# Performance work log

Hardware: AMD Instinct MI355X
Metric: run time of the kernel (lower is better)

Reference implementation:

```python
import jax, jax.numpy as jnp
import numpy as np

N_EMBD = 768
N_HEAD = 12
HEAD_DIM = N_EMBD // N_HEAD


def setup_inputs() -> dict:
    key = jax.random.key(0)
    k1, k2, k3, k4, k5 = jax.random.split(key, 5)
    B, T, C = 8, 1024, N_EMBD
    s = 0.02
    return {
        "x": jax.random.normal(k1, (B, T, C), dtype=jnp.float32),
        "w_attn": jax.random.normal(k2, (C, 3 * C), dtype=jnp.float32) * s,
        "b_attn": jnp.zeros((3 * C,), dtype=jnp.float32),
        "w_proj": jax.random.normal(k3, (C, C), dtype=jnp.float32) * s,
        "b_proj": jnp.zeros((C,), dtype=jnp.float32),
    }


def reference(x, w_attn, b_attn, w_proj, b_proj):
    B, T, C = x.shape
    H, D = N_HEAD, HEAD_DIM
    qkv = x @ w_attn + b_attn                      # [B,T,3C]
    q, k, v = jnp.split(qkv, 3, axis=-1)
    # [B,H,T,D]
    q = q.reshape(B, T, H, D).transpose(0, 2, 1, 3)
    k = k.reshape(B, T, H, D).transpose(0, 2, 1, 3)
    v = v.reshape(B, T, H, D).transpose(0, 2, 1, 3)
    att = jnp.einsum("bhqd,bhkd->bhqk", q, k) / jnp.sqrt(jnp.float32(D))
    causal = jnp.tril(jnp.ones((T, T), dtype=bool))
    att = jnp.where(causal[None, None], att, jnp.float32(-jnp.inf))
    att = jax.nn.softmax(att, axis=-1)
    y = jnp.einsum("bhqk,bhkd->bhqd", att, v)      # [B,H,T,D]
    y = y.transpose(0, 2, 1, 3).reshape(B, T, C)
    return y @ w_proj + b_proj
```

## Files before the change

kernel.cpp:

```cpp
#include <hip/hip_runtime.h>
#include <hip/hip_bf16.h>
#include <math.h>
#include <type_traits>

#define BATCH 8
#define SEQ   1024
#define NEMBD 768
#define NHEAD 12
#define HDIM  64
#define TC    (3 * NEMBD)

typedef __attribute__((ext_vector_type(4))) float f32x4;
typedef __attribute__((ext_vector_type(8))) short s16x8;

__device__ __forceinline__ unsigned short f2bf(float f) {
    return __builtin_bit_cast(unsigned short, __float2bfloat16(f));
}

__device__ __forceinline__ void gload_lds16(const void* g, void* l) {
    __builtin_amdgcn_global_load_lds(
        (const __attribute__((address_space(1))) void*)g,
        (__attribute__((address_space(3))) void*)l, 16, 0, 0);
}

__global__ __launch_bounds__(256) void cast_bf16_kernel(
    const float* __restrict__ in, unsigned short* __restrict__ out, int n)
{
    const int i = (blockIdx.x * 256 + threadIdx.x) * 8;
    float4 a = *(const float4*)(in + i);
    float4 b = *(const float4*)(in + i + 4);
    s16x8 v;
    v[0] = f2bf(a.x); v[1] = f2bf(a.y); v[2] = f2bf(a.z); v[3] = f2bf(a.w);
    v[4] = f2bf(b.x); v[5] = f2bf(b.y); v[6] = f2bf(b.z); v[7] = f2bf(b.w);
    *(s16x8*)(out + i) = v;
}

__global__ __launch_bounds__(256) void transpose_cast_kernel(
    const float* __restrict__ w, unsigned short* __restrict__ wT, int K, int N)
{
    __shared__ float t[32][33];
    const int tx = threadIdx.x, ty = threadIdx.y;
    const int n0 = blockIdx.x * 32, k0 = blockIdx.y * 32;
    #pragma unroll
    for (int i = 0; i < 4; ++i)
        t[ty + i * 8][tx] = w[(size_t)(k0 + ty + i * 8) * N + n0 + tx];
    __syncthreads();
    #pragma unroll
    for (int i = 0; i < 4; ++i)
        wT[(size_t)(n0 + ty + i * 8) * K + k0 + tx] = f2bf(t[tx][ty + i * 8]);
}

__global__ __launch_bounds__(256) void gemm_proj_kernel(
    const unsigned short* __restrict__ A,
    const unsigned short* __restrict__ Bt,
    const float* __restrict__ bias,
    float* __restrict__ C,
    int M, int N, int K, int nbn)
{
    constexpr int BUF = 16384;
    __shared__ __align__(16) char SM[3 * BUF];

    const int tid  = threadIdx.x;
    const int w    = tid >> 6, lane = tid & 63;
    const int lr   = lane & 15, lg = lane >> 4;
    const int wr   = w >> 1, wc = w & 1;

    const int swz = (blockIdx.x & 7) * (gridDim.x >> 3) + (blockIdx.x >> 3);
    const int bm = (swz / nbn) * 128, bn = (swz % nbn) * 128;

    const int srow = tid >> 2;
    const int gcol = ((tid & 3) ^ ((srow >> 1) & 3)) * 8;
    const unsigned short* Ag = A  + (size_t)(bm + srow) * K + gcol;
    const unsigned short* Bg = Bt + (size_t)(bn + srow) * K + gcol;

    const int NT = K >> 5;

    f32x4 acc[4][4];
    #pragma unroll
    for (int m = 0; m < 4; ++m)
        #pragma unroll
        for (int n = 0; n < 4; ++n) acc[m][n] = (f32x4){0.f, 0.f, 0.f, 0.f};

    auto stage = [&](int t) {
        const int k0 = t << 5;
        char* buf = SM + (t % 3) * BUF;
        #pragma unroll
        for (int p = 0; p < 2; ++p)
            gload_lds16(Ag + (size_t)(p * 64) * K + k0, buf + p * 4096 + tid * 16);
        #pragma unroll
        for (int p = 0; p < 2; ++p)
            gload_lds16(Bg + (size_t)(p * 64) * K + k0,
                        buf + 8192 + p * 4096 + tid * 16);
    };

    stage(0);
    stage(1);
    asm volatile("s_waitcnt vmcnt(4)" ::: "memory");
    __builtin_amdgcn_sched_barrier(0);
    __builtin_amdgcn_s_barrier();
    __builtin_amdgcn_sched_barrier(0);

    for (int t = 0; t < NT; ++t) {
        const char* buf = SM + (t % 3) * BUF;
        const bool more = (t + 2 < NT);
        if (more) stage(t + 2);

        s16x8 af[4], bfr[4];
        #pragma unroll
        for (int m = 0; m < 4; ++m) {
            const int ar = wr * 64 + m * 16 + lr;
            af[m] = *(const s16x8*)(buf + ar * 64 + ((lg ^ ((ar >> 1) & 3)) * 16));
        }
        #pragma unroll
        for (int n = 0; n < 4; ++n) {
            const int br = wc * 64 + n * 16 + lr;
            bfr[n] = *(const s16x8*)(buf + 8192 + br * 64
                                         + ((lg ^ ((br >> 1) & 3)) * 16));
        }

        __builtin_amdgcn_s_setprio(1);
        #pragma unroll
        for (int m = 0; m < 4; ++m)
            #pragma unroll
            for (int n = 0; n < 4; ++n)
                acc[m][n] = __builtin_amdgcn_mfma_f32_16x16x32_bf16(
                    af[m], bfr[n], acc[m][n], 0, 0, 0);
        __builtin_amdgcn_s_setprio(0);

        if (more) asm volatile("s_waitcnt vmcnt(4)" ::: "memory");
        else      asm volatile("s_waitcnt vmcnt(0)" ::: "memory");
        __builtin_amdgcn_sched_barrier(0);
        __builtin_amdgcn_s_barrier();
        __builtin_amdgcn_sched_barrier(0);
    }

    #pragma unroll
    for (int n = 0; n < 4; ++n) {
        const int col = bn + wc * 64 + n * 16 + lr;
        const float bv = bias[col];
        #pragma unroll
        for (int m = 0; m < 4; ++m) {
            const int row0 = bm + wr * 64 + m * 16 + lg * 4;
            #pragma unroll
            for (int r = 0; r < 4; ++r)
                C[(size_t)(row0 + r) * N + col] = acc[m][n][r] + bv;
        }
    }
}

__global__ __launch_bounds__(512) void gemm_qkv256_kernel(
    const unsigned short* __restrict__ A,
    const unsigned short* __restrict__ Bt,
    const float* __restrict__ bias,
    unsigned short* __restrict__ Qb,
    unsigned short* __restrict__ Kb,
    unsigned short* __restrict__ Vtb,
    int M, int K, int nbn)
{
    constexpr int BUF = 24576;
    __shared__ __align__(16) char SM[3 * BUF];

    const int tid  = threadIdx.x;
    const int w    = tid >> 6, lane = tid & 63;
    const int lr   = lane & 15, lg = lane >> 4;
    const int wr   = w >> 1, wc = w & 1;

    const int swz = (blockIdx.x & 7) * (gridDim.x >> 3) + (blockIdx.x >> 3);
    const int bm = (swz / nbn) * 256, bn = (swz % nbn) * 128;

    const int srow = tid >> 2;
    const int gcol = ((tid & 3) ^ ((srow >> 1) & 3)) * 8;
    const unsigned short* Ag = A  + (size_t)(bm + srow) * K + gcol;
    const unsigned short* Bg = Bt + (size_t)(bn + srow) * K + gcol;

    const int NT = K >> 5;

    f32x4 acc[4][4];
    #pragma unroll
    for (int m = 0; m < 4; ++m)
        #pragma unroll
        for (int n = 0; n < 4; ++n) acc[m][n] = (f32x4){0.f, 0.f, 0.f, 0.f};

    auto stage = [&](int t) {
        const int k0 = t << 5;
        char* buf = SM + (t % 3) * BUF;
        gload_lds16(Ag + k0,                        buf + tid * 16);
        gload_lds16(Ag + (size_t)128 * K + k0,      buf + 8192 + tid * 16);
        gload_lds16(Bg + k0,                        buf + 16384 + tid * 16);
    };

    stage(0);
    stage(1);
    asm volatile("s_waitcnt vmcnt(3)" ::: "memory");
    __builtin_amdgcn_sched_barrier(0);
    __builtin_amdgcn_s_barrier();
    __builtin_amdgcn_sched_barrier(0);

    for (int t = 0; t < NT; ++t) {
        const char* buf = SM + (t % 3) * BUF;
        const bool more = (t + 2 < NT);
        if (more) stage(t + 2);

        s16x8 af[4], bfr[4];
        #pragma unroll
        for (int m = 0; m < 4; ++m) {
            const int ar = wr * 64 + m * 16 + lr;
            af[m] = *(const s16x8*)(buf + ar * 64 + ((lg ^ ((ar >> 1) & 3)) * 16));
        }
        #pragma unroll
        for (int n = 0; n < 4; ++n) {
            const int br = wc * 64 + n * 16 + lr;
            bfr[n] = *(const s16x8*)(buf + 16384 + br * 64
                                         + ((lg ^ ((br >> 1) & 3)) * 16));
        }

        __builtin_amdgcn_s_setprio(1);
        #pragma unroll
        for (int m = 0; m < 4; ++m)
            #pragma unroll
            for (int n = 0; n < 4; ++n)
                acc[m][n] = __builtin_amdgcn_mfma_f32_16x16x32_bf16(
                    af[m], bfr[n], acc[m][n], 0, 0, 0);
        __builtin_amdgcn_s_setprio(0);

        if (more) asm volatile("s_waitcnt vmcnt(3)" ::: "memory");
        else      asm volatile("s_waitcnt vmcnt(0)" ::: "memory");
        __builtin_amdgcn_sched_barrier(0);
        __builtin_amdgcn_s_barrier();
        __builtin_amdgcn_sched_barrier(0);
    }

    char* Ep = SM + w * 8192;

    const int region = bn / NEMBD;
    const int hh = ((bn % NEMBD) >> 6) + wc;
    const int row0 = bm + wr * 64;
    const int bb = row0 >> 10, t0 = row0 & 1023;
    const float scl = (region == 0) ? 0.1803368801111354f : 1.0f;

    float bvn[4];
    #pragma unroll
    for (int n = 0; n < 4; ++n) bvn[n] = bias[bn + wc * 64 + n * 16 + lr];

    if (region == 2) {
        #pragma unroll
        for (int m = 0; m < 4; ++m)
            #pragma unroll
            for (int n = 0; n < 4; ++n) {
                ushort4 pk;
                pk.x = f2bf(acc[m][n][0] + bvn[n]);
                pk.y = f2bf(acc[m][n][1] + bvn[n]);
                pk.z = f2bf(acc[m][n][2] + bvn[n]);
                pk.w = f2bf(acc[m][n][3] + bvn[n]);
                const int row = n * 16 + lr;
                const int lc  = m * 2 + (lg >> 1);
                *(ushort4*)(Ep + row * 128 + ((lc ^ (lr & 7)) * 16)
                               + (lg & 1) * 8) = pk;
            }
    } else {
        #pragma unroll
        for (int m = 0; m < 4; ++m)
            #pragma unroll
            for (int n = 0; n < 4; ++n)
                #pragma unroll
                for (int r = 0; r < 4; ++r) {
                    const int row = m * 16 + lg * 4 + r;
                    const int lc  = n * 2 + (lr >> 3);
                    *(unsigned short*)(Ep + row * 128
                        + ((lc ^ (row & 7)) * 16) + (lr & 7) * 2) =
                        f2bf((acc[m][n][r] + bvn[n]) * scl);
                }
    }
    asm volatile("s_waitcnt lgkmcnt(0)" ::: "memory");
    __builtin_amdgcn_sched_barrier(0);

    const int rr0 = lane >> 3;
    const int cc  = lane & 7;
    if (region == 2) {
        unsigned short* dst = Vtb + (((size_t)bb * NHEAD + hh) * HDIM) * SEQ + t0;
        #pragma unroll
        for (int it = 0; it < 8; ++it) {
            const int d = it * 8 + rr0;
            s16x8 v = *(const s16x8*)(Ep + d * 128 + ((cc ^ (d & 7)) * 16));
            *(s16x8*)(dst + (size_t)d * SEQ + cc * 8) = v;
        }
    } else {
        unsigned short* dst = (region == 0 ? Qb : Kb)
                            + ((size_t)bb * NHEAD + hh) * SEQ * HDIM;
        #pragma unroll
        for (int it = 0; it < 8; ++it) {
            const int t = it * 8 + rr0;
            s16x8 v = *(const s16x8*)(Ep + t * 128 + ((cc ^ (t & 7)) * 16));
            *(s16x8*)(dst + (size_t)(t0 + t) * HDIM + cc * 8) = v;
        }
    }
}

__global__ __launch_bounds__(256) void attn_mfma_kernel(
    const unsigned short* __restrict__ Qb,
    const unsigned short* __restrict__ Kb,
    const unsigned short* __restrict__ Vtb,
    unsigned short* __restrict__ y)
{
    const int bid  = blockIdx.x;
    const int xcd  = bid & 7;
    const int grp  = bid >> 3;
    const int pair = grp & 7;
    const int bh   = xcd + 8 * (grp >> 3);
    const int b    = bh / NHEAD, h = bh % NHEAD;

    const int tid  = threadIdx.x;
    const int w    = tid >> 6;
    const int lane = tid & 63;
    const int lr   = lane & 15;
    const int lg   = lane >> 4;

    __shared__ __align__(16) unsigned short Ks[64 * 72];
    __shared__ __align__(16) unsigned short Vs[64 * 72];
    __shared__ __align__(16) unsigned short Ps[4][16][72];

    const unsigned short* Kg = Kb  + (size_t)bh * SEQ * HDIM;
    const unsigned short* Vg = Vtb + (size_t)bh * HDIM * SEQ;

    const int sr = tid >> 2;
    const int sc = (tid & 3) * 16;
    const unsigned short* Kgr = Kg + (size_t)sr * HDIM + sc;
    const unsigned short* Vgr = Vg + (size_t)sr * SEQ  + sc;
    unsigned short* KsW = Ks + sr * 72 + sc;
    unsigned short* VsW = Vs + sr * 72 + sc;

    auto process = [&](int qt) {
        const unsigned short* Qg =
            Qb + ((size_t)bh * SEQ + qt * 64 + w * 16) * HDIM;
        s16x8 qf[2];
        #pragma unroll
        for (int kc = 0; kc < 2; ++kc)
            qf[kc] = *(const s16x8*)(Qg + (size_t)lr * HDIM + kc * 32 + lg * 8);

        f32x4 acc[4];
        #pragma unroll
        for (int df = 0; df < 4; ++df) acc[df] = (f32x4){0.f, 0.f, 0.f, 0.f};
        float mrow = -INFINITY, lrow = 0.f;

        const int NT   = qt + 1;
        const int qrow = qt * 64 + w * 16 + lr;

        s16x8 krA = *(const s16x8*)(Kgr);
        s16x8 krB = *(const s16x8*)(Kgr + 8);
        s16x8 vrA = *(const s16x8*)(Vgr);
        s16x8 vrB = *(const s16x8*)(Vgr + 8);

        for (int kt = 0; kt < NT; ++kt) {
            __syncthreads();
            *(s16x8*)(KsW)     = krA;
            *(s16x8*)(KsW + 8) = krB;
            *(s16x8*)(VsW)     = vrA;
            *(s16x8*)(VsW + 8) = vrB;
            __syncthreads();
            if (kt + 1 < NT) {
                krA = *(const s16x8*)(Kgr + (size_t)(kt + 1) * 64 * HDIM);
                krB = *(const s16x8*)(Kgr + (size_t)(kt + 1) * 64 * HDIM + 8);
                vrA = *(const s16x8*)(Vgr + (kt + 1) * 64);
                vrB = *(const s16x8*)(Vgr + (kt + 1) * 64 + 8);
            }

            f32x4 sf[4];
            __builtin_amdgcn_s_setprio(1);
            #pragma unroll
            for (int s = 0; s < 4; ++s) {
                const unsigned short* kr = &Ks[(s * 16 + lr) * 72 + lg * 8];
                s16x8 a0 = *(const s16x8*)(kr);
                s16x8 a1 = *(const s16x8*)(kr + 32);
                sf[s] = __builtin_amdgcn_mfma_f32_16x16x32_bf16(
                    a0, qf[0], (f32x4){0.f, 0.f, 0.f, 0.f}, 0, 0, 0);
                sf[s] = __builtin_amdgcn_mfma_f32_16x16x32_bf16(a1, qf[1], sf[s], 0, 0, 0);
            }
            __builtin_amdgcn_s_setprio(0);

            float sv[4][4];
            #pragma unroll
            for (int s = 0; s < 4; ++s)
                #pragma unroll
                for (int r = 0; r < 4; ++r)
                    sv[s][r] = sf[s][r];
            if (kt == NT - 1) {
                const int kbase = kt * 64;
                #pragma unroll
                for (int s = 0; s < 4; ++s)
                    #pragma unroll
                    for (int r = 0; r < 4; ++r)
                        if (kbase + s * 16 + lg * 4 + r > qrow)
                            sv[s][r] = -INFINITY;
            }

            float mx4[4];
            #pragma unroll
            for (int s = 0; s < 4; ++s)
                mx4[s] = fmaxf(fmaxf(sv[s][0], sv[s][1]), fmaxf(sv[s][2], sv[s][3]));
            float mx = fmaxf(fmaxf(mx4[0], mx4[1]), fmaxf(mx4[2], mx4[3]));
            mx = fmaxf(mx, __shfl_xor(mx, 16, 64));
            mx = fmaxf(mx, __shfl_xor(mx, 32, 64));
            if (!__all(mx - mrow <= 8.f)) {
                const float mnew = fmaxf(mrow, mx);
                const float al   = exp2f(mrow - mnew);
                lrow *= al;
                #pragma unroll
                for (int df = 0; df < 4; ++df) acc[df] *= al;
                mrow = mnew;
            }

            float rsum = 0.f;
            #pragma unroll
            for (int s = 0; s < 4; ++s) {
                float p0 = exp2f(sv[s][0] - mrow);
                float p1 = exp2f(sv[s][1] - mrow);
                float p2 = exp2f(sv[s][2] - mrow);
                float p3 = exp2f(sv[s][3] - mrow);
                rsum += (p0 + p1) + (p2 + p3);
                ushort4 pk;
                pk.x = f2bf(p0); pk.y = f2bf(p1); pk.z = f2bf(p2); pk.w = f2bf(p3);
                *(ushort4*)&Ps[w][lr][s * 16 + lg * 4] = pk;
            }
            rsum += __shfl_xor(rsum, 16, 64);
            rsum += __shfl_xor(rsum, 32, 64);
            lrow += rsum;

            asm volatile("s_waitcnt lgkmcnt(0)" ::: "memory");
            __builtin_amdgcn_sched_barrier(0);
            s16x8 pa[2];
            #pragma unroll
            for (int kc = 0; kc < 2; ++kc)
                pa[kc] = *(const s16x8*)&Ps[w][lr][kc * 32 + lg * 8];

            __builtin_amdgcn_s_setprio(1);
            #pragma unroll
            for (int df = 0; df < 4; ++df) {
                const unsigned short* vr = &Vs[(df * 16 + lr) * 72 + lg * 8];
                s16x8 va0 = *(const s16x8*)(vr);
                s16x8 va1 = *(const s16x8*)(vr + 32);
                acc[df] = __builtin_amdgcn_mfma_f32_16x16x32_bf16(va0, pa[0], acc[df], 0, 0, 0);
                acc[df] = __builtin_amdgcn_mfma_f32_16x16x32_bf16(va1, pa[1], acc[df], 0, 0, 0);
            }
            __builtin_amdgcn_s_setprio(0);
        }

        const float inv = 1.f / lrow;
        const int t = qt * 64 + w * 16 + lr;
        unsigned short* yp = y + ((size_t)(b * SEQ) + t) * NEMBD + h * HDIM;
        #pragma unroll
        for (int df = 0; df < 4; ++df) {
            ushort4 pk;
            pk.x = f2bf(acc[df][0] * inv);
            pk.y = f2bf(acc[df][1] * inv);
            pk.z = f2bf(acc[df][2] * inv);
            pk.w = f2bf(acc[df][3] * inv);
            *(ushort4*)(yp + df * 16 + lg * 4) = pk;
        }
    };

    process(15 - pair);
    process(pair);
}

extern "C" void kernel_launch(void* const* d_in, const int* in_sizes, int n_in,
                              void* d_out, int out_size, void* d_ws, size_t ws_size,
                              hipStream_t stream)
{
    const float* x      = (const float*)d_in[0];
    const float* w_attn = (const float*)d_in[1];
    const float* b_attn = (const float*)d_in[2];
    const float* w_proj = (const float*)d_in[3];
    const float* b_proj = (const float*)d_in[4];
    float* out = (float*)d_out;

    const int M = BATCH * SEQ;
    const size_t NQKV = (size_t)M * NEMBD;

    unsigned short* xb  = (unsigned short*)d_ws;
    unsigned short* waT = xb  + NQKV;
    unsigned short* wpT = waT + (size_t)TC * NEMBD;
    unsigned short* Qb  = wpT + (size_t)NEMBD * NEMBD;
    unsigned short* Kb  = Qb  + NQKV;
    unsigned short* Vtb = Kb  + NQKV;
    unsigned short* yb  = Vtb + NQKV;

    cast_bf16_kernel<<<(M * NEMBD) / 2048, 256, 0, stream>>>(x, xb, M * NEMBD);
    transpose_cast_kernel<<<dim3(TC / 32, NEMBD / 32), dim3(32, 8), 0, stream>>>(
        w_attn, waT, NEMBD, TC);
    transpose_cast_kernel<<<dim3(NEMBD / 32, NEMBD / 32), dim3(32, 8), 0, stream>>>(
        w_proj, wpT, NEMBD, NEMBD);

    gemm_qkv256_kernel<<<(M / 256) * (TC / 128), 512, 0, stream>>>(
        xb, waT, b_attn, Qb, Kb, Vtb, M, NEMBD, TC / 128);

    attn_mfma_kernel<<<768, 256, 0, stream>>>(Qb, Kb, Vtb, yb);

    gemm_proj_kernel<<<(NEMBD / 128) * (M / 128), 256, 0, stream>>>(
        yb, wpT, b_proj, out, M, NEMBD, NEMBD, NEMBD / 128);
}
```

Before: 109.6 us.

## Use square 256x256 tiles with double buffering in QKV GEMM

The QKV projection GEMM tile grows from 256x128 to 256x256. The 8 waves are rearranged as 2x4, each computing 128x64, and the triple-buffered LDS pipeline becomes a double-buffered one with the wait placed before compute. The goal is more operand reuse per LDS load and fewer global loads of the weight matrix. The costs are half as many blocks (288, close to one wave on the device), a doubled accumulator register count that pressures occupancy, and less load/compute overlap from the shallower pipeline.

```diff
diff --git a/kernel.cpp b/kernel.cpp
--- a/kernel.cpp
+++ b/kernel.cpp
@@ -148,7 +148,7 @@
     }
 }
 
-__global__ __launch_bounds__(512) void gemm_qkv256_kernel(
+__global__ __launch_bounds__(512, 2) void gemm_qkv256sq_kernel(
     const unsigned short* __restrict__ A,
     const unsigned short* __restrict__ Bt,
     const float* __restrict__ bias,
@@ -157,16 +157,16 @@
     unsigned short* __restrict__ Vtb,
     int M, int K, int nbn)
 {
-    constexpr int BUF = 24576;
-    __shared__ __align__(16) char SM[3 * BUF];
+    constexpr int BUF = 32768;
+    __shared__ __align__(16) char SM[2 * BUF];
 
     const int tid  = threadIdx.x;
     const int w    = tid >> 6, lane = tid & 63;
     const int lr   = lane & 15, lg = lane >> 4;
-    const int wr   = w >> 1, wc = w & 1;
+    const int wr   = w >> 2, wc = w & 3;
 
     const int swz = (blockIdx.x & 7) * (gridDim.x >> 3) + (blockIdx.x >> 3);
-    const int bm = (swz / nbn) * 256, bn = (swz % nbn) * 128;
+    const int bm = (swz / nbn) * 256, bn = (swz % nbn) * 256;
 
     const int srow = tid >> 2;
     const int gcol = ((tid & 3) ^ ((srow >> 1) & 3)) * 8;
@@ -175,36 +175,36 @@
 
     const int NT = K >> 5;
 
-    f32x4 acc[4][4];
-    #pragma unroll
-    for (int m = 0; m < 4; ++m)
+    f32x4 acc[8][4];
+    #pragma unroll
+    for (int m = 0; m < 8; ++m)
         #pragma unroll
         for (int n = 0; n < 4; ++n) acc[m][n] = (f32x4){0.f, 0.f, 0.f, 0.f};
 
     auto stage = [&](int t) {
         const int k0 = t << 5;
-        char* buf = SM + (t % 3) * BUF;
-        gload_lds16(Ag + k0,                        buf + tid * 16);
-        gload_lds16(Ag + (size_t)128 * K + k0,      buf + 8192 + tid * 16);
-        gload_lds16(Bg + k0,                        buf + 16384 + tid * 16);
+        char* buf = SM + (t & 1) * BUF;
+        gload_lds16(Ag + k0,                   buf + tid * 16);
+        gload_lds16(Ag + (size_t)128 * K + k0, buf + 8192 + tid * 16);
+        gload_lds16(Bg + k0,                   buf + 16384 + tid * 16);
+        gload_lds16(Bg + (size_t)128 * K + k0, buf + 24576 + tid * 16);
     };
 
     stage(0);
-    stage(1);
-    asm volatile("s_waitcnt vmcnt(3)" ::: "memory");
-    __builtin_amdgcn_sched_barrier(0);
-    __builtin_amdgcn_s_barrier();
-    __builtin_amdgcn_sched_barrier(0);
-
     for (int t = 0; t < NT; ++t) {
-        const char* buf = SM + (t % 3) * BUF;
-        const bool more = (t + 2 < NT);
-        if (more) stage(t + 2);
-
-        s16x8 af[4], bfr[4];
-        #pragma unroll
-        for (int m = 0; m < 4; ++m) {
-            const int ar = wr * 64 + m * 16 + lr;
+        const bool more = (t + 1 < NT);
+        if (more) stage(t + 1);
+        if (more) asm volatile("s_waitcnt vmcnt(4)" ::: "memory");
+        else      asm volatile("s_waitcnt vmcnt(0)" ::: "memory");
+        __builtin_amdgcn_sched_barrier(0);
+        __builtin_amdgcn_s_barrier();
+        __builtin_amdgcn_sched_barrier(0);
+
+        const char* buf = SM + (t & 1) * BUF;
+        s16x8 af[8], bfr[4];
+        #pragma unroll
+        for (int m = 0; m < 8; ++m) {
+            const int ar = wr * 128 + m * 16 + lr;
             af[m] = *(const s16x8*)(buf + ar * 64 + ((lg ^ ((ar >> 1) & 3)) * 16));
         }
         #pragma unroll
@@ -216,15 +216,13 @@
 
         __builtin_amdgcn_s_setprio(1);
         #pragma unroll
-        for (int m = 0; m < 4; ++m)
+        for (int m = 0; m < 8; ++m)
             #pragma unroll
             for (int n = 0; n < 4; ++n)
                 acc[m][n] = __builtin_amdgcn_mfma_f32_16x16x32_bf16(
                     af[m], bfr[n], acc[m][n], 0, 0, 0);
         __builtin_amdgcn_s_setprio(0);
 
-        if (more) asm volatile("s_waitcnt vmcnt(3)" ::: "memory");
-        else      asm volatile("s_waitcnt vmcnt(0)" ::: "memory");
         __builtin_amdgcn_sched_barrier(0);
         __builtin_amdgcn_s_barrier();
         __builtin_amdgcn_sched_barrier(0);
@@ -234,64 +232,73 @@
 
     const int region = bn / NEMBD;
     const int hh = ((bn % NEMBD) >> 6) + wc;
-    const int row0 = bm + wr * 64;
-    const int bb = row0 >> 10, t0 = row0 & 1023;
     const float scl = (region == 0) ? 0.1803368801111354f : 1.0f;
 
     float bvn[4];
     #pragma unroll
     for (int n = 0; n < 4; ++n) bvn[n] = bias[bn + wc * 64 + n * 16 + lr];
 
-    if (region == 2) {
-        #pragma unroll
-        for (int m = 0; m < 4; ++m)
-            #pragma unroll
-            for (int n = 0; n < 4; ++n) {
-                ushort4 pk;
-                pk.x = f2bf(acc[m][n][0] + bvn[n]);
-                pk.y = f2bf(acc[m][n][1] + bvn[n]);
-                pk.z = f2bf(acc[m][n][2] + bvn[n]);
-                pk.w = f2bf(acc[m][n][3] + bvn[n]);
-                const int row = n * 16 + lr;
-                const int lc  = m * 2 + (lg >> 1);
-                *(ushort4*)(Ep + row * 128 + ((lc ^ (lr & 7)) * 16)
-                               + (lg & 1) * 8) = pk;
-            }
-    } else {
-        #pragma unroll
-        for (int m = 0; m < 4; ++m)
-            #pragma unroll
-            for (int n = 0; n < 4; ++n)
+    #pragma unroll
+    for (int c = 0; c < 2; ++c) {
+        if (c) {
+            asm volatile("s_waitcnt lgkmcnt(0)" ::: "memory");
+            __builtin_amdgcn_sched_barrier(0);
+        }
+        const int row0 = bm + wr * 128 + c * 64;
+        const int bb = row0 >> 10, t0 = row0 & 1023;
+
+        if (region == 2) {
+            #pragma unroll
+            for (int m4 = 0; m4 < 4; ++m4)
                 #pragma unroll
-                for (int r = 0; r < 4; ++r) {
-                    const int row = m * 16 + lg * 4 + r;
-                    const int lc  = n * 2 + (lr >> 3);
-                    *(unsigned short*)(Ep + row * 128
-                        + ((lc ^ (row & 7)) * 16) + (lr & 7) * 2) =
-                        f2bf((acc[m][n][r] + bvn[n]) * scl);
+                for (int n = 0; n < 4; ++n) {
+                    const f32x4 a = acc[c * 4 + m4][n];
+                    ushort4 pk;
+                    pk.x = f2bf(a[0] + bvn[n]);
+                    pk.y = f2bf(a[1] + bvn[n]);
+                    pk.z = f2bf(a[2] + bvn[n]);
+                    pk.w = f2bf(a[3] + bvn[n]);
+                    const int row = n * 16 + lr;
+                    const int lc  = m4 * 2 + (lg >> 1);
+                    *(ushort4*)(Ep + row * 128 + ((lc ^ (lr & 7)) * 16)
+                                   + (lg & 1) * 8) = pk;
                 }
-    }
-    asm volatile("s_waitcnt lgkmcnt(0)" ::: "memory");
-    __builtin_amdgcn_sched_barrier(0);
-
-    const int rr0 = lane >> 3;
-    const int cc  = lane & 7;
-    if (region == 2) {
-        unsigned short* dst = Vtb + (((size_t)bb * NHEAD + hh) * HDIM) * SEQ + t0;
-        #pragma unroll
-        for (int it = 0; it < 8; ++it) {
-            const int d = it * 8 + rr0;
-            s16x8 v = *(const s16x8*)(Ep + d * 128 + ((cc ^ (d & 7)) * 16));
-            *(s16x8*)(dst + (size_t)d * SEQ + cc * 8) = v;
-        }
-    } else {
-        unsigned short* dst = (region == 0 ? Qb : Kb)
-                            + ((size_t)bb * NHEAD + hh) * SEQ * HDIM;
-        #pragma unroll
-        for (int it = 0; it < 8; ++it) {
-            const int t = it * 8 + rr0;
-            s16x8 v = *(const s16x8*)(Ep + t * 128 + ((cc ^ (t & 7)) * 16));
-            *(s16x8*)(dst + (size_t)(t0 + t) * HDIM + cc * 8) = v;
+        } else {
+            #pragma unroll
+            for (int m4 = 0; m4 < 4; ++m4)
+                #pragma unroll
+                for (int n = 0; n < 4; ++n)
+                    #pragma unroll
+                    for (int r = 0; r < 4; ++r) {
+                        const int row = m4 * 16 + lg * 4 + r;
+                        const int lc  = n * 2 + (lr >> 3);
+                        *(unsigned short*)(Ep + row * 128
+                            + ((lc ^ (row & 7)) * 16) + (lr & 7) * 2) =
+                            f2bf((acc[c * 4 + m4][n][r] + bvn[n]) * scl);
+                    }
+        }
+        asm volatile("s_waitcnt lgkmcnt(0)" ::: "memory");
+        __builtin_amdgcn_sched_barrier(0);
+
+        const int rr0 = lane >> 3;
+        const int cc  = lane & 7;
+        if (region == 2) {
+            unsigned short* dst = Vtb + (((size_t)bb * NHEAD + hh) * HDIM) * SEQ + t0;
+            #pragma unroll
+            for (int it = 0; it < 8; ++it) {
+                const int d = it * 8 + rr0;
+                s16x8 v = *(const s16x8*)(Ep + d * 128 + ((cc ^ (d & 7)) * 16));
+                *(s16x8*)(dst + (size_t)d * SEQ + cc * 8) = v;
+            }
+        } else {
+            unsigned short* dst = (region == 0 ? Qb : Kb)
+                                + ((size_t)bb * NHEAD + hh) * SEQ * HDIM;
+            #pragma unroll
+            for (int it = 0; it < 8; ++it) {
+                const int t = it * 8 + rr0;
+                s16x8 v = *(const s16x8*)(Ep + t * 128 + ((cc ^ (t & 7)) * 16));
+                *(s16x8*)(dst + (size_t)(t0 + t) * HDIM + cc * 8) = v;
+            }
         }
     }
 }
@@ -490,8 +497,8 @@
     transpose_cast_kernel<<<dim3(NEMBD / 32, NEMBD / 32), dim3(32, 8), 0, stream>>>(
         w_proj, wpT, NEMBD, NEMBD);
 
-    gemm_qkv256_kernel<<<(M / 256) * (TC / 128), 512, 0, stream>>>(
-        xb, waT, b_attn, Qb, Kb, Vtb, M, NEMBD, TC / 128);
+    gemm_qkv256sq_kernel<<<(M / 256) * (TC / 256), 512, 0, stream>>>(
+        xb, waT, b_attn, Qb, Kb, Vtb, M, NEMBD, TC / 256);
 
     attn_mfma_kernel<<<768, 256, 0, stream>>>(Qb, Kb, Vtb, yb);
 
```

Measured after the change: 119.2 us. 1.09x slower.
